# Performance work log

Hardware: AMD Instinct MI355X
Metric: run time of the kernel (lower is better)

Reference implementation:

```python
import jax, jax.numpy as jnp
import numpy as np

EPS = 1e-5  # torch LayerNorm default eps

def _layernorm(x):
    mu = x.mean(axis=-1, keepdims=True)
    var = x.var(axis=-1, keepdims=True)  # biased, matches torch
    return (x - mu) / jnp.sqrt(var + EPS)

def setup_inputs() -> dict:
    key = jax.random.key(0)
    k1, k2, k3, k4, k5 = jax.random.split(key, 5)
    B, T, E, H = 8, 2048, 512, 8
    d = E // H
    return {
        "input1": jax.random.normal(k1, (B, T, E), dtype=jnp.float32),
        "Wq": jax.random.normal(k2, (H, d), dtype=jnp.float32) * 0.1,
        "Wk": jax.random.normal(k3, (H, d), dtype=jnp.float32) * 0.1,
        "Wv": jax.random.normal(k4, (H, d, d), dtype=jnp.float32) * 0.1,
        "Wm": jax.random.normal(k5, (E, E), dtype=jnp.float32) * 0.05,
    }

def reference(input1, Wq, Wk, Wv, Wm):
    B, T, E = input1.shape
    H, d = Wq.shape
    xn = _layernorm(input1)                       # norm1 over Embed_Dim
    xh = xn.reshape(B, T, H, d)                   # per-head slices of last dim
    # QLayer surrogates: scalar query/key per token, d-dim value per token
    Q = jnp.einsum('bthd,hd->bht', xh, Wq)        # [B,H,T]
    K = jnp.einsum('bthd,hd->bht', xh, Wk)        # [B,H,T]
    V = jnp.einsum('bthd,hde->bhte', xh, Wv)      # [B,H,T,d]
    # distance attention: A = -(Q_i - K_j)^2
    A = -(Q[:, :, :, None] - K[:, :, None, :]) ** 2   # [B,H,T,T]
    P = jax.nn.softmax(A / (d ** 0.5), axis=-1)
    O = jnp.einsum('bhts,bhse->bhte', P, V)       # [B,H,T,d]
    head_result = O.transpose(0, 2, 1, 3).reshape(B, T, E)  # concat heads
    return head_result @ Wm + input1              # merger + residual
```

## Files before the change

kernel.cpp:

```cpp
#include <hip/hip_runtime.h>

typedef __bf16 bf16x8 __attribute__((ext_vector_type(8)));
typedef short short8 __attribute__((ext_vector_type(8)));
typedef float f32x4 __attribute__((ext_vector_type(4)));

#define TT 2048
#define EE 512
#define NH 8
#define DD 64

#define QSCALE 0.36067376022224085f
#define CSCALE 0.18033688011112042f

__device__ __forceinline__ ushort f2bf(float f) {
  union { float f; unsigned u; } a; a.f = f;
  unsigned u = a.u;
  return (ushort)((u + 0x7FFFu + ((u >> 16) & 1u)) >> 16);
}

__global__ __launch_bounds__(1024) void k_lnt(
    const float* __restrict__ x, const float* __restrict__ Wq,
    const float* __restrict__ Wk,
    float* __restrict__ Q, float* __restrict__ K, ushort* __restrict__ xnt) {
  const int tid = threadIdx.x;
  const int wv = tid >> 6, l = tid & 63;
  const int t0 = blockIdx.x * 64;
  __shared__ ushort tile[64][520];

#pragma unroll
  for (int it = 0; it < 4; it++) {
    const int tl = wv * 4 + it;
    const int token = t0 + tl;
    const float* xr = x + (size_t)token * EE + l * 8;
    float4 a = *(const float4*)xr;
    float4 c = *(const float4*)(xr + 4);
    float xv[8] = {a.x, a.y, a.z, a.w, c.x, c.y, c.z, c.w};
    float s = 0.f, s2 = 0.f;
#pragma unroll
    for (int i = 0; i < 8; i++) { s += xv[i]; s2 = fmaf(xv[i], xv[i], s2); }
#pragma unroll
    for (int o = 32; o; o >>= 1) { s += __shfl_xor(s, o); s2 += __shfl_xor(s2, o); }
    const float mean = s * (1.f / 512.f);
    const float var = s2 * (1.f / 512.f) - mean * mean;
    const float rstd = rsqrtf(var + 1e-5f);

    float xn[8];
    short8 ob;
#pragma unroll
    for (int i = 0; i < 8; i++) {
      xn[i] = (xv[i] - mean) * rstd;
      ob[i] = (short)f2bf(xn[i]);
    }
    *(short8*)&tile[tl][l * 8] = ob;

    const float* wq = Wq + l * 8;
    const float* wk = Wk + l * 8;
    float4 q1 = *(const float4*)wq, q2 = *(const float4*)(wq + 4);
    float4 k1 = *(const float4*)wk, k2 = *(const float4*)(wk + 4);
    float wqv[8] = {q1.x, q1.y, q1.z, q1.w, q2.x, q2.y, q2.z, q2.w};
    float wkv[8] = {k1.x, k1.y, k1.z, k1.w, k2.x, k2.y, k2.z, k2.w};
    float q = 0.f, k = 0.f;
#pragma unroll
    for (int i = 0; i < 8; i++) { q = fmaf(xn[i], wqv[i], q); k = fmaf(xn[i], wkv[i], k); }
#pragma unroll
    for (int o = 4; o; o >>= 1) { q += __shfl_xor(q, o); k += __shfl_xor(k, o); }
    if ((l & 7) == 0) {
      const int h = l >> 3;
      const int b = token >> 11, t = token & (TT - 1);
      const int bh = b * NH + h;
      Q[bh * TT + t] = q * QSCALE;
      K[bh * TT + t] = k;
    }
  }
  __syncthreads();

  {
    const int h = tid >> 7, e = (tid >> 1) & 63, half = tid & 1;
    const int b = t0 >> 11, trow = t0 & (TT - 1);
    const int col = h * 64 + e;
    ushort* rowp = xnt + (size_t)((b * NH + h) * DD + e) * TT + trow;
#pragma unroll
    for (int ch = 0; ch < 4; ch++) {
      const int c_idx = half * 4 + ch;
      union { uint4 v; ushort u[8]; } o;
#pragma unroll
      for (int i = 0; i < 8; i++) o.u[i] = tile[c_idx * 8 + i][col];
      *(uint4*)(rowp + (((c_idx ^ (e & 7)) << 3))) = o.v;
    }
  }
}

__global__ __launch_bounds__(256) void k_wvm(
    const float* __restrict__ Wv, const float* __restrict__ Wm,
    ushort* __restrict__ Wvmt) {
  const int k = blockIdx.x;
  const int h = k >> 6;
  const int tid = threadIdx.x;
  __shared__ float wv[64];
  if (tid < 64) wv[tid] = Wv[k * 64 + tid];
  __syncthreads();
  float a0 = 0.f, a1 = 0.f;
#pragma unroll 8
  for (int e = 0; e < 64; e++) {
    const float w = wv[e];
    const float* row = Wm + (size_t)(h * 64 + e) * EE;
    a0 = fmaf(w, row[tid], a0);
    a1 = fmaf(w, row[tid + 256], a1);
  }
  Wvmt[(size_t)tid * EE + k] = f2bf(a0);
  Wvmt[(size_t)(tid + 256) * EE + k] = f2bf(a1);
}

__global__ __launch_bounds__(256, 2) void k_attn(
    const float* __restrict__ Q, const float* __restrict__ K,
    const ushort* __restrict__ xnt, ushort* __restrict__ hr) {
  const int sw = (blockIdx.x & 7) * 64 + (blockIdx.x >> 3);
  const int bh = sw >> 3;
  const int q0 = (sw & 7) * 256;
  const int b = bh >> 3, h = bh & 7;
  const int tid = threadIdx.x;
  const int w = tid >> 6, l = tid & 63;
  const int l16 = l & 15, lhi = l >> 4;

  __shared__ float ks[TT];
  __shared__ float cs[TT];
  __shared__ ushort vt[2][64 * 64];

  {
    const float* Kb = K + bh * TT;
#pragma unroll
    for (int i = 0; i < 8; i++) {
      float kv = Kb[tid + i * 256];
      ks[tid + i * 256] = kv;
      cs[tid + i * 256] = -kv * kv * CSCALE;
    }
  }

  const ushort* Xs = xnt + (size_t)bh * (DD * TT);
  const int se = tid >> 3;
  const int sc = (tid & 7) * 8;
  uint4 st0, st1;

#define ISSUE_STAGE(jt_) do {                                                  \
    st0 = *(const uint4*)(Xs + (size_t)se * TT + (jt_) + sc);                  \
    st1 = *(const uint4*)(Xs + (size_t)(se + 32) * TT + (jt_) + sc);           \
  } while (0)

#define WRITE_STAGE(buf_) do {                                                 \
    *(uint4*)&vt[buf_][se * 64 + sc] = st0;                                    \
    *(uint4*)&vt[buf_][(se + 32) * 64 + sc] = st1;                             \
  } while (0)

  ISSUE_STAGE(0);
  WRITE_STAGE(0);
  __syncthreads();

  float qv[4];
#pragma unroll
  for (int f = 0; f < 4; f++) qv[f] = Q[bh * TT + q0 + w * 64 + f * 16 + l16];

  f32x4 acc[4][4];
  f32x4 accd[4];
#pragma unroll
  for (int f = 0; f < 4; f++) {
    accd[f] = (f32x4){0.f, 0.f, 0.f, 0.f};
#pragma unroll
    for (int c = 0; c < 4; c++) acc[f][c] = (f32x4){0.f, 0.f, 0.f, 0.f};
  }
  short8 onesbits = {0x3F80, 0x3F80, 0x3F80, 0x3F80, 0x3F80, 0x3F80, 0x3F80, 0x3F80};
  const bf16x8 ones = __builtin_bit_cast(bf16x8, onesbits);

  int p = 0;
  for (int jt = 0; jt < TT; jt += 64) {
    const bool more = (jt + 64) < TT;
    if (more) ISSUE_STAGE(jt + 64);

    __builtin_amdgcn_s_setprio(1);
#pragma unroll
    for (int kk = 0; kk < 2; kk++) {
      bf16x8 vf[4];
#pragma unroll
      for (int c = 0; c < 4; c++) {
        const int e = c * 16 + l16;
        vf[c] = *(const bf16x8*)&vt[p][e * 64 + (((kk * 4 + lhi) ^ (e & 7)) << 3)];
      }
      const int jb = jt + kk * 32 + lhi * 8;
      float4 ka = *(const float4*)&ks[jb];
      float4 kb2 = *(const float4*)&ks[jb + 4];
      float4 ca = *(const float4*)&cs[jb];
      float4 cb2 = *(const float4*)&cs[jb + 4];
      float kv8[8] = {ka.x, ka.y, ka.z, ka.w, kb2.x, kb2.y, kb2.z, kb2.w};
      float cv8[8] = {ca.x, ca.y, ca.z, ca.w, cb2.x, cb2.y, cb2.z, cb2.w};
#pragma unroll
      for (int f = 0; f < 4; f++) {
        bf16x8 pa;
#pragma unroll
        for (int i = 0; i < 8; i++)
          pa[i] = (__bf16)__builtin_amdgcn_exp2f(fmaf(qv[f], kv8[i], cv8[i]));
        accd[f] = __builtin_amdgcn_mfma_f32_16x16x32_bf16(pa, ones, accd[f], 0, 0, 0);
#pragma unroll
        for (int c = 0; c < 4; c++)
          acc[f][c] = __builtin_amdgcn_mfma_f32_16x16x32_bf16(pa, vf[c], acc[f][c], 0, 0, 0);
      }
    }
    __builtin_amdgcn_s_setprio(0);

    if (more) WRITE_STAGE(p ^ 1);
    __syncthreads();
    p ^= 1;
  }
#undef ISSUE_STAGE
#undef WRITE_STAGE

#pragma unroll
  for (int f = 0; f < 4; f++) {
#pragma unroll
    for (int r = 0; r < 4; r++) {
      const float rinv = 1.f / accd[f][r];
      const int qrow = q0 + w * 64 + f * 16 + lhi * 4 + r;
      const size_t base = ((size_t)(b * TT + qrow)) * EE + h * DD + l16;
#pragma unroll
      for (int c = 0; c < 4; c++)
        hr[base + c * 16] = f2bf(acc[f][c][r] * rinv);
    }
  }
}

__global__ __launch_bounds__(256, 2) void k_merge(
    const ushort* __restrict__ hr, const ushort* __restrict__ Wmt,
    const float* __restrict__ x, float* __restrict__ out) {
  const int fid = blockIdx.y * 4 + blockIdx.x;
  const int xcd = fid & 7, idx = fid >> 3;
  const int n0 = (idx & 3) * 128;
  const int m0 = (xcd * 16 + (idx >> 2)) * 128;
  const int tid = threadIdx.x;
  const int w = tid >> 6, l = tid & 63;
  const int l16 = l & 15, lhi = l >> 4;
  const int wm = w >> 1, wn = w & 1;

  __shared__ ushort As[2][128 * 72];
  __shared__ ushort Bs[2][128 * 72];
  f32x4 acc[4][4];
#pragma unroll
  for (int i = 0; i < 4; i++)
#pragma unroll
    for (int j = 0; j < 4; j++) acc[i][j] = (f32x4){0.f, 0.f, 0.f, 0.f};

  const int row = tid >> 1, half = tid & 1;
  const ushort* sa0 = hr + (size_t)(m0 + row) * EE + half * 32;
  const ushort* sb0 = Wmt + (size_t)(n0 + row) * EE + half * 32;

  {
    uint4* da = (uint4*)&As[0][row * 72 + half * 32];
    uint4* db = (uint4*)&Bs[0][row * 72 + half * 32];
#pragma unroll
    for (int i = 0; i < 4; i++) da[i] = *(const uint4*)(sa0 + i * 8);
#pragma unroll
    for (int i = 0; i < 4; i++) db[i] = *(const uint4*)(sb0 + i * 8);
  }
  __syncthreads();

  int p = 0;
  for (int k0 = 0; k0 < EE; k0 += 64) {
    const bool more = (k0 + 64) < EE;
    uint4 pa[4], pb[4];
    if (more) {
#pragma unroll
      for (int i = 0; i < 4; i++) pa[i] = *(const uint4*)(sa0 + k0 + 64 + i * 8);
#pragma unroll
      for (int i = 0; i < 4; i++) pb[i] = *(const uint4*)(sb0 + k0 + 64 + i * 8);
    }
#pragma unroll
    for (int kk = 0; kk < 2; kk++) {
      bf16x8 af[4], bfr[4];
#pragma unroll
      for (int mi = 0; mi < 4; mi++)
        af[mi] = *(const bf16x8*)&As[p][(wm * 64 + mi * 16 + l16) * 72 + kk * 32 + lhi * 8];
#pragma unroll
      for (int ni = 0; ni < 4; ni++)
        bfr[ni] = *(const bf16x8*)&Bs[p][(wn * 64 + ni * 16 + l16) * 72 + kk * 32 + lhi * 8];
#pragma unroll
      for (int mi = 0; mi < 4; mi++)
#pragma unroll
        for (int ni = 0; ni < 4; ni++)
          acc[mi][ni] = __builtin_amdgcn_mfma_f32_16x16x32_bf16(af[mi], bfr[ni], acc[mi][ni], 0, 0, 0);
    }
    if (more) {
      uint4* da = (uint4*)&As[p ^ 1][row * 72 + half * 32];
      uint4* db = (uint4*)&Bs[p ^ 1][row * 72 + half * 32];
#pragma unroll
      for (int i = 0; i < 4; i++) da[i] = pa[i];
#pragma unroll
      for (int i = 0; i < 4; i++) db[i] = pb[i];
    }
    __syncthreads();
    p ^= 1;
  }

#pragma unroll
  for (int mi = 0; mi < 4; mi++) {
#pragma unroll
    for (int r = 0; r < 4; r++) {
      const int grow = m0 + wm * 64 + mi * 16 + lhi * 4 + r;
#pragma unroll
      for (int ni = 0; ni < 4; ni++) {
        const int gcol = n0 + wn * 64 + ni * 16 + l16;
        size_t idx2 = (size_t)grow * EE + gcol;
        out[idx2] = acc[mi][ni][r] + x[idx2];
      }
    }
  }
}

extern "C" void kernel_launch(void* const* d_in, const int* in_sizes, int n_in,
                              void* d_out, int out_size, void* d_ws, size_t ws_size,
                              hipStream_t stream) {
  const float* x  = (const float*)d_in[0];
  const float* Wq = (const float*)d_in[1];
  const float* Wk = (const float*)d_in[2];
  const float* Wv = (const float*)d_in[3];
  const float* Wm = (const float*)d_in[4];
  float* out = (float*)d_out;

  char* ws = (char*)d_ws;
  float*  Qp   = (float*)(ws);
  float*  Kp   = (float*)(ws + 524288);
  ushort* hrp  = (ushort*)(ws + 1048576);
  ushort* xnt  = (ushort*)(ws + 17825792);
  ushort* Wvmt = (ushort*)(ws + 34603008);

  k_lnt<<<256, 1024, 0, stream>>>(x, Wq, Wk, Qp, Kp, xnt);
  k_wvm<<<EE, 256, 0, stream>>>(Wv, Wm, Wvmt);
  k_attn<<<512, 256, 0, stream>>>(Qp, Kp, xnt, hrp);
  k_merge<<<dim3(EE / 128, (8 * TT) / 128), 256, 0, stream>>>(hrp, Wvmt, x, out);
}
```

Before: 119.2 us.

## Split key tiles across wave pairs and double attention grid

Each attention block now handles 128 queries instead of 256. Pairs of waves split each 64-key tile between them and merge their partial numerators and denominators through shared memory at the end. The grid doubles and the occupancy hint rises to 3 blocks per CU, to expose more parallelism and latency hiding. In exchange, K and V staging is repeated by twice as many blocks, and an extra reduction with barriers is added in the epilogue.

Result: slower. 124.6 us (+4.6%).

```diff
diff --git a/kernel.cpp b/kernel.cpp
--- a/kernel.cpp
+++ b/kernel.cpp
@@ -111,20 +111,23 @@
   Wvmt[(size_t)(tid + 256) * EE + k] = f2bf(a1);
 }
 
-__global__ __launch_bounds__(256, 2) void k_attn(
+__global__ __launch_bounds__(256, 3) void k_attn(
     const float* __restrict__ Q, const float* __restrict__ K,
     const ushort* __restrict__ xnt, ushort* __restrict__ hr) {
-  const int sw = (blockIdx.x & 7) * 64 + (blockIdx.x >> 3);
-  const int bh = sw >> 3;
-  const int q0 = (sw & 7) * 256;
+  const int sw = (blockIdx.x & 7) * 128 + (blockIdx.x >> 3);
+  const int bh = sw >> 4;
+  const int q0 = (sw & 15) * 128;
   const int b = bh >> 3, h = bh & 7;
   const int tid = threadIdx.x;
   const int w = tid >> 6, l = tid & 63;
   const int l16 = l & 15, lhi = l >> 4;
-
-  __shared__ float ks[TT];
-  __shared__ float cs[TT];
-  __shared__ ushort vt[2][64 * 64];
+  const int qg = w >> 1;
+  const int kkw = w & 1;
+
+  __shared__ float smemf[8192];
+  float* ks = smemf;
+  float* cs = smemf + 2048;
+  ushort* vt = (ushort*)(smemf + 4096);
 
   {
     const float* Kb = K + bh * TT;
@@ -147,8 +150,8 @@
   } while (0)
 
 #define WRITE_STAGE(buf_) do {                                                 \
-    *(uint4*)&vt[buf_][se * 64 + sc] = st0;                                    \
-    *(uint4*)&vt[buf_][(se + 32) * 64 + sc] = st1;                             \
+    *(uint4*)&vt[(buf_) * 4096 + se * 64 + sc] = st0;                          \
+    *(uint4*)&vt[(buf_) * 4096 + (se + 32) * 64 + sc] = st1;                   \
   } while (0)
 
   ISSUE_STAGE(0);
@@ -157,7 +160,7 @@
 
   float qv[4];
 #pragma unroll
-  for (int f = 0; f < 4; f++) qv[f] = Q[bh * TT + q0 + w * 64 + f * 16 + l16];
+  for (int f = 0; f < 4; f++) qv[f] = Q[bh * TT + q0 + qg * 64 + f * 16 + l16];
 
   f32x4 acc[4][4];
   f32x4 accd[4];
@@ -176,15 +179,14 @@
     if (more) ISSUE_STAGE(jt + 64);
 
     __builtin_amdgcn_s_setprio(1);
-#pragma unroll
-    for (int kk = 0; kk < 2; kk++) {
+    {
       bf16x8 vf[4];
 #pragma unroll
       for (int c = 0; c < 4; c++) {
         const int e = c * 16 + l16;
-        vf[c] = *(const bf16x8*)&vt[p][e * 64 + (((kk * 4 + lhi) ^ (e & 7)) << 3)];
+        vf[c] = *(const bf16x8*)&vt[p * 4096 + e * 64 + (((kkw * 4 + lhi) ^ (e & 7)) << 3)];
       }
-      const int jb = jt + kk * 32 + lhi * 8;
+      const int jb = jt + kkw * 32 + lhi * 8;
       float4 ka = *(const float4*)&ks[jb];
       float4 kb2 = *(const float4*)&ks[jb + 4];
       float4 ca = *(const float4*)&cs[jb];
@@ -212,16 +214,48 @@
 #undef ISSUE_STAGE
 #undef WRITE_STAGE
 
-#pragma unroll
-  for (int f = 0; f < 4; f++) {
-#pragma unroll
-    for (int r = 0; r < 4; r++) {
-      const float rinv = 1.f / accd[f][r];
-      const int qrow = q0 + w * 64 + f * 16 + lhi * 4 + r;
-      const size_t base = ((size_t)(b * TT + qrow)) * EE + h * DD + l16;
+  float* cb = smemf;
+  if (kkw == 1) {
+#pragma unroll
+    for (int f = 0; f < 4; f++)
 #pragma unroll
       for (int c = 0; c < 4; c++)
-        hr[base + c * 16] = f2bf(acc[f][c][r] * rinv);
+#pragma unroll
+        for (int r = 0; r < 4; r++)
+          cb[qg * 4096 + (f * 16 + c * 4 + r) * 64 + l] = acc[f][c][r];
+  }
+  __syncthreads();
+  if (kkw == 0) {
+#pragma unroll
+    for (int f = 0; f < 4; f++)
+#pragma unroll
+      for (int c = 0; c < 4; c++)
+#pragma unroll
+        for (int r = 0; r < 4; r++)
+          acc[f][c][r] += cb[qg * 4096 + (f * 16 + c * 4 + r) * 64 + l];
+  }
+  __syncthreads();
+  if (kkw == 1) {
+#pragma unroll
+    for (int f = 0; f < 4; f++)
+#pragma unroll
+      for (int r = 0; r < 4; r++)
+        cb[qg * 1024 + (f * 4 + r) * 64 + l] = accd[f][r];
+  }
+  __syncthreads();
+  if (kkw == 0) {
+#pragma unroll
+    for (int f = 0; f < 4; f++) {
+#pragma unroll
+      for (int r = 0; r < 4; r++) {
+        const float rs = accd[f][r] + cb[qg * 1024 + (f * 4 + r) * 64 + l];
+        const float rinv = 1.f / rs;
+        const int qrow = q0 + qg * 64 + f * 16 + lhi * 4 + r;
+        const size_t base = ((size_t)(b * TT + qrow)) * EE + h * DD + l16;
+#pragma unroll
+        for (int c = 0; c < 4; c++)
+          hr[base + c * 16] = f2bf(acc[f][c][r] * rinv);
+      }
     }
   }
 }
@@ -331,6 +365,6 @@
 
   k_lnt<<<256, 1024, 0, stream>>>(x, Wq, Wk, Qp, Kp, xnt);
   k_wvm<<<EE, 256, 0, stream>>>(Wv, Wm, Wvmt);
-  k_attn<<<512, 256, 0, stream>>>(Qp, Kp, xnt, hrp);
+  k_attn<<<1024, 256, 0, stream>>>(Qp, Kp, xnt, hrp);
   k_merge<<<dim3(EE / 128, (8 * TT) / 128), 256, 0, stream>>>(hrp, Wvmt, x, out);
 }
```
